# Performance work log

Measured on AMD Instinct MI355X. Metric: run time of the kernel, lower is better.

Reference implementation:

```python
import jax, jax.numpy as jnp
import numpy as np

N = 10000   # num_nodes (batch=1)
E = 160000  # num edges
CIN, H, T, OUT, K = 32, 64, 12, 12, 3


def _conv1d(x, w, b, pad):
    # x: [N, C_in, T], w: [C_out, C_in, K]
    out = jax.lax.conv_general_dilated(
        x, w, window_strides=(1,), padding=[(pad, pad)],
        dimension_numbers=('NCH', 'OIH', 'NCH'))
    return out + b[None, :, None]


def _gated_tconv(x, w, b):
    # GatedTemporalConv (dropout = identity in eval)
    out = _conv1d(x, w, b, K // 2)
    P, Q = jnp.split(out, 2, axis=1)
    return P * jax.nn.sigmoid(Q)


def _gcn(x, W, b, src, dst, ew):
    # PyG GCNConv, vectorized over all T timesteps in one fused pass.
    # x: [N, C_in, T], W: [C_out, C_in]
    xt = jnp.einsum('nct,oc->not', x, W)
    loop = jnp.arange(N)
    srcl = jnp.concatenate([src, loop])
    dstl = jnp.concatenate([dst, loop])
    ewl = jnp.concatenate([ew, jnp.ones((N,), ew.dtype)])
    deg = jax.ops.segment_sum(ewl, dstl, num_segments=N)
    dis = jnp.where(deg > 0, jax.lax.rsqrt(deg), 0.0)
    norm = dis[srcl] * ewl * dis[dstl]                      # [E+N]
    msg = xt[srcl] * norm[:, None, None]                    # [E+N, C_out, T]
    out = jax.ops.segment_sum(msg, dstl, num_segments=N)    # [N, C_out, T]
    return out + b[None, :, None]


def setup_inputs() -> dict:
    key = jax.random.key(0)
    ks = jax.random.split(key, 20)
    rn = lambda k, s: jax.random.normal(k, s, jnp.float32) * 0.05
    return {
        'x': jax.random.normal(ks[0], (N, CIN, T), jnp.float32),
        'edge_index': jax.random.randint(ks[1], (2, E), 0, N),
        'edge_weight': jax.random.uniform(ks[2], (E,), jnp.float32),
        'tc1a_w': rn(ks[3], (2 * H, CIN, K)), 'tc1a_b': rn(ks[4], (2 * H,)),
        'gc1_w': rn(ks[5], (H, H)),           'gc1_b': rn(ks[6], (H,)),
        'tc1b_w': rn(ks[7], (2 * H, H, K)),   'tc1b_b': rn(ks[8], (2 * H,)),
        'tc2a_w': rn(ks[9], (2 * H, H, K)),   'tc2a_b': rn(ks[10], (2 * H,)),
        'gc2_w': rn(ks[11], (H, H)),          'gc2_b': rn(ks[12], (H,)),
        'tc2b_w': rn(ks[13], (2 * H, H, K)),  'tc2b_b': rn(ks[14], (2 * H,)),
        'fin_w': rn(ks[15], (OUT, H, T)),     'fin_b': rn(ks[16], (OUT,)),
    }


def reference(x, edge_index, edge_weight,
              tc1a_w, tc1a_b, gc1_w, gc1_b, tc1b_w, tc1b_b,
              tc2a_w, tc2a_b, gc2_w, gc2_b, tc2b_w, tc2b_b,
              fin_w, fin_b):
    src, dst = edge_index[0], edge_index[1]
    h = _gated_tconv(x, tc1a_w, tc1a_b)
    h = jax.nn.relu(_gcn(h, gc1_w, gc1_b, src, dst, edge_weight))
    h = _gated_tconv(h, tc1b_w, tc1b_b)
    h = _gated_tconv(h, tc2a_w, tc2a_b)
    h = jax.nn.relu(_gcn(h, gc2_w, gc2_b, src, dst, edge_weight))
    h = _gated_tconv(h, tc2b_w, tc2b_b)
    h = _conv1d(h, fin_w, fin_b, 0)          # [N, OUT, 1] (kernel == T)
    h = h[:, :, 0]                            # squeeze(-1)
    return h.reshape(1, N, OUT)               # batch_size = 1
```

## Files before the change

kernel.cpp:

```cpp
#include <hip/hip_runtime.h>
#include <hip/hip_bf16.h>
#include <stdint.h>

#define N_NODES 10000
#define N_EDGES 160000

typedef unsigned short u16;
typedef unsigned int u32;
typedef short s16v8 __attribute__((ext_vector_type(8)));
typedef float f32v4 __attribute__((ext_vector_type(4)));

__device__ __forceinline__ float bf2f(u16 v){ return __uint_as_float(((u32)v) << 16); }
__device__ __forceinline__ float lo16(u32 u){ return __uint_as_float(u << 16); }
__device__ __forceinline__ float hi16(u32 u){ return __uint_as_float(u & 0xffff0000u); }
__device__ __forceinline__ u16 f2bf(float f){
    u32 u = __float_as_uint(f);
    u32 r = (u + 0x7fffu + ((u >> 16) & 1u)) >> 16;
    return (u16)r;
}
__device__ __forceinline__ u32 pack2(float a, float b){
    return (u32)f2bf(a) | ((u32)f2bf(b) << 16);
}

struct SmallPtrs { const void* p[14]; };

__device__ __constant__ const int g_seg_off[15] = {
    0, 12288, 12416, 16512, 16576, 41152, 41280,
    65856, 65984, 70080, 70144, 94720, 94848, 104064, 104076
};

__global__ void k_convert_init(SmallPtrs ps, u16* __restrict__ dst,
                               float* deg, int* cnt, int* cur){
    int i = blockIdx.x * blockDim.x + threadIdx.x;
    if (i < 104076){
        int seg = 0, base = 0;
#pragma unroll
        for (int s = 0; s < 14; s++){
            if (i >= g_seg_off[s]){ seg = s; base = g_seg_off[s]; }
        }
        dst[i] = f2bf(((const float*)ps.p[seg])[i - base]);
    }
    if (i < N_NODES){ deg[i] = 1.0f; cnt[i] = 0; cur[i] = 0; }
}

__global__ void k_graph_count(const int* __restrict__ ei, const float* __restrict__ ew,
                              float* deg, int* cnt){
    int e = blockIdx.x * blockDim.x + threadIdx.x;
    if (e < N_EDGES){
        int d = ei[N_EDGES + e];
        atomicAdd(&deg[d], ew[e]);
        atomicAdd(&cnt[d], 1);
    }
}

__global__ void k_scan_dis(const int* __restrict__ cnt, int* __restrict__ off,
                           const float* __restrict__ deg, float* __restrict__ dis){
    __shared__ int wsum[16], woff[16];
    int t = threadIdx.x;
    int lane = t & 63, wv = t >> 6;
    int base = t * 10;
    int loc[10];
    int mysum = 0;
    if (base < N_NODES){
#pragma unroll
        for (int j = 0; j < 10; j++){ loc[j] = mysum; mysum += cnt[base + j]; }
    }
    int s = mysum;
#pragma unroll
    for (int d = 1; d < 64; d <<= 1){
        int v = __shfl_up(s, d, 64);
        if (lane >= d) s += v;
    }
    if (lane == 63) wsum[wv] = s;
    __syncthreads();
    if (t < 16){
        int v = wsum[t];
        int sc = v;
#pragma unroll
        for (int d = 1; d < 16; d <<= 1){
            int u = __shfl_up(sc, d, 16);
            if (t >= d) sc += u;
        }
        woff[t] = sc - v;
        if (t == 15) off[N_NODES] = sc;
    }
    __syncthreads();
    int tbase = woff[wv] + (s - mysum);
    if (base < N_NODES){
#pragma unroll
        for (int j = 0; j < 10; j++) off[base + j] = tbase + loc[j];
    }
    for (int i = t; i < N_NODES; i += 1024) dis[i] = rsqrtf(deg[i]);
}

__global__ void k_scatter(const int* __restrict__ ei, const float* __restrict__ ew,
                          const float* __restrict__ dis, const int* __restrict__ off,
                          int* cur, int* __restrict__ esrc, float* __restrict__ enorm){
    int e = blockIdx.x * blockDim.x + threadIdx.x;
    if (e < N_EDGES){
        int s = ei[e];
        int d = ei[N_EDGES + e];
        float nw = dis[s] * ew[e] * dis[d];
        int p = off[d] + atomicAdd(&cur[d], 1);
        esrc[p] = s;
        enorm[p] = nw;
    }
}

__launch_bounds__(256, 2)
__global__ void k_gconv32(const float* __restrict__ xin, const u16* __restrict__ wg,
                          const u16* __restrict__ bg, u16* __restrict__ out){
    __shared__ __attribute__((aligned(16))) u16 xT[8][14][40];
    __shared__ __attribute__((aligned(16))) u16 Ho[8][12][72];
    int tid = threadIdx.x;
    int n0 = blockIdx.x * 8;

    for (int i = tid; i < 8 * 40; i += 256){
        int g = i / 40, c = i % 40;
        xT[g][0][c] = 0; xT[g][13][c] = 0;
    }
    {
        int g = tid >> 5, c = tid & 31;
        const float4* p = (const float4*)(xin + ((size_t)(n0 + g) * 32 + c) * 12);
        float4 v0 = p[0], v1 = p[1], v2 = p[2];
        xT[g][1][c] = f2bf(v0.x);  xT[g][2][c] = f2bf(v0.y);
        xT[g][3][c] = f2bf(v0.z);  xT[g][4][c] = f2bf(v0.w);
        xT[g][5][c] = f2bf(v1.x);  xT[g][6][c] = f2bf(v1.y);
        xT[g][7][c] = f2bf(v1.z);  xT[g][8][c] = f2bf(v1.w);
        xT[g][9][c] = f2bf(v2.x);  xT[g][10][c] = f2bf(v2.y);
        xT[g][11][c] = f2bf(v2.z); xT[g][12][c] = f2bf(v2.w);
    }
    int lane = tid & 63, wave = tid >> 6;
    int col = lane & 15, quad = lane >> 4;
    int o_p = wave * 16 + col, o_q = o_p + 64;

    s16v8 Bf[3][2];
#pragma unroll
    for (int pq = 0; pq < 2; pq++){
        const u16* wrow = wg + (size_t)(pq ? o_q : o_p) * 96;
#pragma unroll
        for (int d = 0; d < 3; d++){
            s16v8 b;
#pragma unroll
            for (int j = 0; j < 8; j++) b[j] = (short)wrow[(quad * 8 + j) * 3 + d];
            Bf[d][pq] = b;
        }
    }
    __syncthreads();

    f32v4 aP[6], aQ[6];
#pragma unroll
    for (int mt = 0; mt < 6; mt++){ aP[mt] = (f32v4)0.f; aQ[mt] = (f32v4)0.f; }
#pragma unroll
    for (int mt = 0; mt < 6; mt++){
        int m = mt * 16 + col;
        int g = m / 12, t = m - 12 * g;
#pragma unroll
        for (int d = 0; d < 3; d++){
            s16v8 a = *(const s16v8*)&xT[g][t + d][quad * 8];
            aP[mt] = __builtin_amdgcn_mfma_f32_16x16x32_bf16(a, Bf[d][0], aP[mt], 0, 0, 0);
            aQ[mt] = __builtin_amdgcn_mfma_f32_16x16x32_bf16(a, Bf[d][1], aQ[mt], 0, 0, 0);
        }
    }
    float bP = bf2f(bg[o_p]), bQ = bf2f(bg[o_q]);
#pragma unroll
    for (int mt = 0; mt < 6; mt++){
#pragma unroll
        for (int r = 0; r < 4; r++){
            int m2 = mt * 16 + quad * 4 + r;
            int g = m2 / 12, t = m2 - 12 * g;
            float pv = aP[mt][r] + bP, qv = aQ[mt][r] + bQ;
            Ho[g][t][o_p] = f2bf(pv / (1.f + __expf(-qv)));
        }
    }
    __syncthreads();
    for (int i = tid; i < 768; i += 256){
        int g = i / 96, r = i % 96, t = r / 8, ch = r % 8;
        *(s16v8*)(out + (size_t)(n0 + g) * 768 + t * 64 + ch * 8) = *(const s16v8*)&Ho[g][t][ch * 8];
    }
}

__global__ void k_agg(const u16* __restrict__ x, u16* __restrict__ out,
                      const float* __restrict__ dis, const int* __restrict__ off,
                      const int* __restrict__ esrc, const float* __restrict__ enorm){
    int n = blockIdx.x;
    int v0 = threadIdx.x * 4;
    float d = dis[n];
    float sw = d * d;
    const u16* xr = x + (size_t)n * 768 + v0;
    u32 u0 = *(const u32*)xr;
    u32 u1 = *(const u32*)(xr + 2);
    float a0 = sw * lo16(u0), a1 = sw * hi16(u0);
    float a2 = sw * lo16(u1), a3 = sw * hi16(u1);
    int b = off[n], e = off[n + 1];
    for (int p = b; p < e; p++){
        int s = esrc[p];
        float w = enorm[p];
        const u16* q = x + (size_t)s * 768 + v0;
        u32 w0 = *(const u32*)q;
        u32 w1 = *(const u32*)(q + 2);
        a0 = fmaf(w, lo16(w0), a0); a1 = fmaf(w, hi16(w0), a1);
        a2 = fmaf(w, lo16(w1), a2); a3 = fmaf(w, hi16(w1), a3);
    }
    u16* o = out + (size_t)n * 768 + v0;
    *(u32*)o       = pack2(a0, a1);
    *(u32*)(o + 2) = pack2(a2, a3);
}

#define XIDX(g, row, c) (((g) * 14 + (row)) * 72 + (c))

template<bool LAST>
__launch_bounds__(256, 2)
__global__ void k_fused(const u16* __restrict__ z,
                        const u16* __restrict__ Wmix, const u16* __restrict__ bmix,
                        const u16* __restrict__ w1, const u16* __restrict__ b1,
                        const u16* __restrict__ w2, const u16* __restrict__ b2,
                        const u16* __restrict__ fw, const u16* __restrict__ fb,
                        u16* __restrict__ outMid, float* __restrict__ outFin){
    __shared__ __attribute__((aligned(16))) u16 bufX[8 * 14 * 72];
    __shared__ __attribute__((aligned(16))) u16 bufY[8 * 14 * 72];
    int tid = threadIdx.x;
    int n0 = blockIdx.x * 8;
    int lane = tid & 63, wave = tid >> 6;
    int col = lane & 15, quad = lane >> 4;

    for (int i = tid; i < 8 * 72; i += 256){
        int g = i / 72, c = i % 72;
        bufX[XIDX(g, 0, c)] = 0; bufX[XIDX(g, 13, c)] = 0;
        bufY[XIDX(g, 0, c)] = 0; bufY[XIDX(g, 13, c)] = 0;
    }
    for (int i = tid; i < 768; i += 256){
        int g = i / 96, r = i % 96, t = r / 8, ch = r % 8;
        *(s16v8*)&bufX[XIDX(g, 1 + t, ch * 8)] =
            *(const s16v8*)(z + (size_t)(n0 + g) * 768 + t * 64 + ch * 8);
    }
    int o_mix = wave * 16 + col;
    s16v8 Bm[2];
#pragma unroll
    for (int ks = 0; ks < 2; ks++)
        Bm[ks] = *(const s16v8*)(Wmix + (size_t)o_mix * 64 + ks * 32 + quad * 8);
    __syncthreads();

    {
        f32v4 accm[6];
#pragma unroll
        for (int mt = 0; mt < 6; mt++) accm[mt] = (f32v4)0.f;
#pragma unroll
        for (int mt = 0; mt < 6; mt++){
            int m = mt * 16 + col;
            int g = m / 12, t = m - 12 * g;
#pragma unroll
            for (int ks = 0; ks < 2; ks++){
                s16v8 a = *(const s16v8*)&bufX[XIDX(g, 1 + t, ks * 32 + quad * 8)];
                accm[mt] = __builtin_amdgcn_mfma_f32_16x16x32_bf16(a, Bm[ks], accm[mt], 0, 0, 0);
            }
        }
        float bm = bf2f(bmix[o_mix]);
#pragma unroll
        for (int mt = 0; mt < 6; mt++){
#pragma unroll
            for (int r = 0; r < 4; r++){
                int m2 = mt * 16 + quad * 4 + r;
                int g = m2 / 12, t = m2 - 12 * g;
                bufY[XIDX(g, 1 + t, o_mix)] = f2bf(fmaxf(accm[mt][r] + bm, 0.f));
            }
        }
    }
    __syncthreads();

    {
        int o_p = wave * 16 + col, o_q = o_p + 64;
        s16v8 Bf[3][2][2];
#pragma unroll
        for (int pq = 0; pq < 2; pq++){
            const u16* wrow = w1 + (size_t)(pq ? o_q : o_p) * 192;
#pragma unroll
            for (int d = 0; d < 3; d++)
#pragma unroll
                for (int ks = 0; ks < 2; ks++){
                    s16v8 b;
#pragma unroll
                    for (int j = 0; j < 8; j++) b[j] = (short)wrow[(ks * 32 + quad * 8 + j) * 3 + d];
                    Bf[d][ks][pq] = b;
                }
        }
        f32v4 aP[6], aQ[6];
#pragma unroll
        for (int mt = 0; mt < 6; mt++){ aP[mt] = (f32v4)0.f; aQ[mt] = (f32v4)0.f; }
#pragma unroll
        for (int mt = 0; mt < 6; mt++){
            int m = mt * 16 + col;
            int g = m / 12, t = m - 12 * g;
#pragma unroll
            for (int d = 0; d < 3; d++)
#pragma unroll
                for (int ks = 0; ks < 2; ks++){
                    s16v8 a = *(const s16v8*)&bufY[XIDX(g, t + d, ks * 32 + quad * 8)];
                    aP[mt] = __builtin_amdgcn_mfma_f32_16x16x32_bf16(a, Bf[d][ks][0], aP[mt], 0, 0, 0);
                    aQ[mt] = __builtin_amdgcn_mfma_f32_16x16x32_bf16(a, Bf[d][ks][1], aQ[mt], 0, 0, 0);
                }
        }
        float bP = bf2f(b1[o_p]), bQ = bf2f(b1[o_q]);
#pragma unroll
        for (int mt = 0; mt < 6; mt++){
#pragma unroll
            for (int r = 0; r < 4; r++){
                int m2 = mt * 16 + quad * 4 + r;
                int g = m2 / 12, t = m2 - 12 * g;
                float pv = aP[mt][r] + bP, qv = aQ[mt][r] + bQ;
                u16 hv = f2bf(pv / (1.f + __expf(-qv)));
                if (LAST) bufX[g * 1008 + o_p * 12 + t] = hv;
                else      bufX[XIDX(g, 1 + t, o_p)] = hv;
            }
        }
    }
    __syncthreads();

    if (!LAST){
        int o_p = wave * 16 + col, o_q = o_p + 64;
        s16v8 Bf[3][2][2];
#pragma unroll
        for (int pq = 0; pq < 2; pq++){
            const u16* wrow = w2 + (size_t)(pq ? o_q : o_p) * 192;
#pragma unroll
            for (int d = 0; d < 3; d++)
#pragma unroll
                for (int ks = 0; ks < 2; ks++){
                    s16v8 b;
#pragma unroll
                    for (int j = 0; j < 8; j++) b[j] = (short)wrow[(ks * 32 + quad * 8 + j) * 3 + d];
                    Bf[d][ks][pq] = b;
                }
        }
        f32v4 aP[6], aQ[6];
#pragma unroll
        for (int mt = 0; mt < 6; mt++){ aP[mt] = (f32v4)0.f; aQ[mt] = (f32v4)0.f; }
#pragma unroll
        for (int mt = 0; mt < 6; mt++){
            int m = mt * 16 + col;
            int g = m / 12, t = m - 12 * g;
#pragma unroll
            for (int d = 0; d < 3; d++)
#pragma unroll
                for (int ks = 0; ks < 2; ks++){
                    s16v8 a = *(const s16v8*)&bufX[XIDX(g, t + d, ks * 32 + quad * 8)];
                    aP[mt] = __builtin_amdgcn_mfma_f32_16x16x32_bf16(a, Bf[d][ks][0], aP[mt], 0, 0, 0);
                    aQ[mt] = __builtin_amdgcn_mfma_f32_16x16x32_bf16(a, Bf[d][ks][1], aQ[mt], 0, 0, 0);
                }
        }
        float bP = bf2f(b2[o_p]), bQ = bf2f(b2[o_q]);
#pragma unroll
        for (int mt = 0; mt < 6; mt++){
#pragma unroll
            for (int r = 0; r < 4; r++){
                int m2 = mt * 16 + quad * 4 + r;
                int g = m2 / 12, t = m2 - 12 * g;
                float pv = aP[mt][r] + bP, qv = aQ[mt][r] + bQ;
                bufY[XIDX(g, 1 + t, o_p)] = f2bf(pv / (1.f + __expf(-qv)));
            }
        }
        __syncthreads();
        for (int i = tid; i < 768; i += 256){
            int g = i / 96, r = i % 96, t = r / 8, ch = r % 8;
            *(s16v8*)(outMid + (size_t)(n0 + g) * 768 + t * 64 + ch * 8) =
                *(const s16v8*)&bufY[XIDX(g, 1 + t, ch * 8)];
        }
    } else {
        if (wave == 0){
            f32v4 accF = {0.f, 0.f, 0.f, 0.f};
            int g8 = col & 7;
#pragma unroll
            for (int ks = 0; ks < 24; ks++){
                s16v8 a = *(const s16v8*)&bufX[g8 * 1008 + ks * 32 + quad * 8];
                s16v8 bfr = {0, 0, 0, 0, 0, 0, 0, 0};
                if (col < 12)
                    bfr = *(const s16v8*)(fw + (size_t)col * 768 + ks * 32 + quad * 8);
                accF = __builtin_amdgcn_mfma_f32_16x16x32_bf16(a, bfr, accF, 0, 0, 0);
            }
            if (col < 12){
                float bb = bf2f(fb[col]);
#pragma unroll
                for (int r = 0; r < 4; r++){
                    int g = quad * 4 + r;
                    if (g < 8) outFin[(size_t)(n0 + g) * 12 + col] = accF[r] + bb;
                }
            }
        }
    }
}

static inline size_t align256(size_t x){ return (x + 255) & ~(size_t)255; }

extern "C" void kernel_launch(void* const* d_in, const int* in_sizes, int n_in,
                              void* d_out, int out_size, void* d_ws, size_t ws_size,
                              hipStream_t stream){
    const float* x  = (const float*)d_in[0];
    const int* ei   = (const int*)d_in[1];
    const float* ew = (const float*)d_in[2];

    char* w = (char*)d_ws;
    u16* bufA    = (u16*)w;  w += align256((size_t)N_NODES * 768 * sizeof(u16));
    u16* bufB    = (u16*)w;  w += align256((size_t)N_NODES * 768 * sizeof(u16));
    float* deg   = (float*)w; w += align256(N_NODES * sizeof(float));
    float* dis   = (float*)w; w += align256(N_NODES * sizeof(float));
    int* cnt     = (int*)w;   w += align256(N_NODES * sizeof(int));
    int* off     = (int*)w;   w += align256((N_NODES + 1) * sizeof(int));
    int* cur     = (int*)w;   w += align256(N_NODES * sizeof(int));
    int* esrc    = (int*)w;   w += align256((size_t)N_EDGES * sizeof(int));
    float* enorm = (float*)w; w += align256((size_t)N_EDGES * sizeof(float));
    u16* cvt     = (u16*)w;   w += align256(104076 * sizeof(u16));

    u16* tc1a_w = cvt + 0;
    u16* tc1a_b = cvt + 12288;
    u16* gc1_w  = cvt + 12416;
    u16* gc1_b  = cvt + 16512;
    u16* tc1b_w = cvt + 16576;
    u16* tc1b_b = cvt + 41152;
    u16* tc2a_w = cvt + 41280;
    u16* tc2a_b = cvt + 65856;
    u16* gc2_w  = cvt + 65984;
    u16* gc2_b  = cvt + 70080;
    u16* tc2b_w = cvt + 70144;
    u16* tc2b_b = cvt + 94720;
    u16* fin_w  = cvt + 94848;
    u16* fin_b  = cvt + 104064;

    SmallPtrs ps;
    ps.p[0]  = d_in[3];  ps.p[1]  = d_in[4];
    ps.p[2]  = d_in[5];  ps.p[3]  = d_in[6];
    ps.p[4]  = d_in[7];  ps.p[5]  = d_in[8];
    ps.p[6]  = d_in[9];  ps.p[7]  = d_in[10];
    ps.p[8]  = d_in[11]; ps.p[9]  = d_in[12];
    ps.p[10] = d_in[13]; ps.p[11] = d_in[14];
    ps.p[12] = d_in[15]; ps.p[13] = d_in[16];

    k_convert_init<<<(104076 + 255) / 256, 256, 0, stream>>>(ps, cvt, deg, cnt, cur);
    k_graph_count<<<(N_EDGES + 255) / 256, 256, 0, stream>>>(ei, ew, deg, cnt);
    k_scan_dis<<<1, 1024, 0, stream>>>(cnt, off, deg, dis);
    k_scatter<<<(N_EDGES + 255) / 256, 256, 0, stream>>>(ei, ew, dis, off, cur, esrc, enorm);

    k_gconv32<<<1250, 256, 0, stream>>>(x, tc1a_w, tc1a_b, bufA);
    k_agg<<<N_NODES, 192, 0, stream>>>(bufA, bufB, dis, off, esrc, enorm);
    k_fused<false><<<1250, 256, 0, stream>>>(bufB, gc1_w, gc1_b, tc1b_w, tc1b_b,
                                             tc2a_w, tc2a_b, nullptr, nullptr,
                                             bufA, nullptr);
    k_agg<<<N_NODES, 192, 0, stream>>>(bufA, bufB, dis, off, esrc, enorm);
    k_fused<true><<<1250, 256, 0, stream>>>(bufB, gc2_w, gc2_b, tc2b_w, tc2b_b,
                                            nullptr, nullptr, fin_w, fin_b,
                                            nullptr, (float*)d_out);
}
```

Measured before the change: 274.3 us.

## Fuse graph aggregation into fused conv kernels and merge count with first conv

Removes the separate k_agg kernels and performs the neighbor aggregation at the start of each k_fused block, writing the aggregated rows straight into shared memory and skipping a global round-trip. The degree counting is merged into the first gated conv launch as extra blocks, and edge source and weight are packed into int2. The conv weights are pre-transposed at conversion time so each B fragment loads as one vector. The cost is lower aggregation parallelism, since one thread now gathers 24 contiguous values per node. Register pressure also rises in k_fused.

Measured after the change: 266.6 us. -2.8%, faster.

```diff
diff --git a/kernel.cpp b/kernel.cpp
--- a/kernel.cpp
+++ b/kernel.cpp
@@ -11,22 +11,20 @@
 typedef float f32v4 __attribute__((ext_vector_type(4)));
 
 __device__ __forceinline__ float bf2f(u16 v){ return __uint_as_float(((u32)v) << 16); }
-__device__ __forceinline__ float lo16(u32 u){ return __uint_as_float(u << 16); }
-__device__ __forceinline__ float hi16(u32 u){ return __uint_as_float(u & 0xffff0000u); }
 __device__ __forceinline__ u16 f2bf(float f){
     u32 u = __float_as_uint(f);
     u32 r = (u + 0x7fffu + ((u >> 16) & 1u)) >> 16;
     return (u16)r;
 }
-__device__ __forceinline__ u32 pack2(float a, float b){
-    return (u32)f2bf(a) | ((u32)f2bf(b) << 16);
-}
 
 struct SmallPtrs { const void* p[14]; };
 
 __device__ __constant__ const int g_seg_off[15] = {
     0, 12288, 12416, 16512, 16576, 41152, 41280,
     65856, 65984, 70080, 70144, 94720, 94848, 104064, 104076
+};
+__device__ __constant__ const int g_seg_kind[14] = {
+    1, 0, 0, 0, 2, 0, 2, 0, 0, 0, 2, 0, 0, 0
 };
 
 __global__ void k_convert_init(SmallPtrs ps, u16* __restrict__ dst,
@@ -38,78 +36,36 @@
         for (int s = 0; s < 14; s++){
             if (i >= g_seg_off[s]){ seg = s; base = g_seg_off[s]; }
         }
-        dst[i] = f2bf(((const float*)ps.p[seg])[i - base]);
+        int li = i - base;
+        float v = ((const float*)ps.p[seg])[li];
+        int kind = g_seg_kind[seg];
+        int dsto = li;
+        if (kind){
+            int CIN = (kind == 1) ? 32 : 64;
+            int o = li / (3 * CIN);
+            int rem = li - o * (3 * CIN);
+            int c = rem / 3, d = rem - c * 3;
+            dsto = d * 128 * CIN + o * CIN + c;
+        }
+        dst[base + dsto] = f2bf(v);
     }
     if (i < N_NODES){ deg[i] = 1.0f; cnt[i] = 0; cur[i] = 0; }
 }
 
-__global__ void k_graph_count(const int* __restrict__ ei, const float* __restrict__ ew,
+__launch_bounds__(256, 2)
+__global__ void k_gconv_count(const float* __restrict__ xin, const u16* __restrict__ wg,
+                              const u16* __restrict__ bg, u16* __restrict__ out,
+                              const int* __restrict__ ei, const float* __restrict__ ew,
                               float* deg, int* cnt){
-    int e = blockIdx.x * blockDim.x + threadIdx.x;
-    if (e < N_EDGES){
-        int d = ei[N_EDGES + e];
-        atomicAdd(&deg[d], ew[e]);
-        atomicAdd(&cnt[d], 1);
-    }
-}
-
-__global__ void k_scan_dis(const int* __restrict__ cnt, int* __restrict__ off,
-                           const float* __restrict__ deg, float* __restrict__ dis){
-    __shared__ int wsum[16], woff[16];
-    int t = threadIdx.x;
-    int lane = t & 63, wv = t >> 6;
-    int base = t * 10;
-    int loc[10];
-    int mysum = 0;
-    if (base < N_NODES){
-#pragma unroll
-        for (int j = 0; j < 10; j++){ loc[j] = mysum; mysum += cnt[base + j]; }
-    }
-    int s = mysum;
-#pragma unroll
-    for (int d = 1; d < 64; d <<= 1){
-        int v = __shfl_up(s, d, 64);
-        if (lane >= d) s += v;
-    }
-    if (lane == 63) wsum[wv] = s;
-    __syncthreads();
-    if (t < 16){
-        int v = wsum[t];
-        int sc = v;
-#pragma unroll
-        for (int d = 1; d < 16; d <<= 1){
-            int u = __shfl_up(sc, d, 16);
-            if (t >= d) sc += u;
-        }
-        woff[t] = sc - v;
-        if (t == 15) off[N_NODES] = sc;
-    }
-    __syncthreads();
-    int tbase = woff[wv] + (s - mysum);
-    if (base < N_NODES){
-#pragma unroll
-        for (int j = 0; j < 10; j++) off[base + j] = tbase + loc[j];
-    }
-    for (int i = t; i < N_NODES; i += 1024) dis[i] = rsqrtf(deg[i]);
-}
-
-__global__ void k_scatter(const int* __restrict__ ei, const float* __restrict__ ew,
-                          const float* __restrict__ dis, const int* __restrict__ off,
-                          int* cur, int* __restrict__ esrc, float* __restrict__ enorm){
-    int e = blockIdx.x * blockDim.x + threadIdx.x;
-    if (e < N_EDGES){
-        int s = ei[e];
-        int d = ei[N_EDGES + e];
-        float nw = dis[s] * ew[e] * dis[d];
-        int p = off[d] + atomicAdd(&cur[d], 1);
-        esrc[p] = s;
-        enorm[p] = nw;
-    }
-}
-
-__launch_bounds__(256, 2)
-__global__ void k_gconv32(const float* __restrict__ xin, const u16* __restrict__ wg,
-                          const u16* __restrict__ bg, u16* __restrict__ out){
+    if (blockIdx.x >= 1250){
+        int e = (blockIdx.x - 1250) * 256 + threadIdx.x;
+        if (e < N_EDGES){
+            int d = ei[N_EDGES + e];
+            atomicAdd(&deg[d], ew[e]);
+            atomicAdd(&cnt[d], 1);
+        }
+        return;
+    }
     __shared__ __attribute__((aligned(16))) u16 xT[8][14][40];
     __shared__ __attribute__((aligned(16))) u16 Ho[8][12][72];
     int tid = threadIdx.x;
@@ -137,14 +93,10 @@
     s16v8 Bf[3][2];
 #pragma unroll
     for (int pq = 0; pq < 2; pq++){
-        const u16* wrow = wg + (size_t)(pq ? o_q : o_p) * 96;
-#pragma unroll
-        for (int d = 0; d < 3; d++){
-            s16v8 b;
-#pragma unroll
-            for (int j = 0; j < 8; j++) b[j] = (short)wrow[(quad * 8 + j) * 3 + d];
-            Bf[d][pq] = b;
-        }
+        int o = pq ? o_q : o_p;
+#pragma unroll
+        for (int d = 0; d < 3; d++)
+            Bf[d][pq] = *(const s16v8*)(wg + d * 4096 + o * 32 + quad * 8);
     }
     __syncthreads();
 
@@ -180,38 +132,66 @@
     }
 }
 
-__global__ void k_agg(const u16* __restrict__ x, u16* __restrict__ out,
-                      const float* __restrict__ dis, const int* __restrict__ off,
-                      const int* __restrict__ esrc, const float* __restrict__ enorm){
-    int n = blockIdx.x;
-    int v0 = threadIdx.x * 4;
-    float d = dis[n];
-    float sw = d * d;
-    const u16* xr = x + (size_t)n * 768 + v0;
-    u32 u0 = *(const u32*)xr;
-    u32 u1 = *(const u32*)(xr + 2);
-    float a0 = sw * lo16(u0), a1 = sw * hi16(u0);
-    float a2 = sw * lo16(u1), a3 = sw * hi16(u1);
-    int b = off[n], e = off[n + 1];
-    for (int p = b; p < e; p++){
-        int s = esrc[p];
-        float w = enorm[p];
-        const u16* q = x + (size_t)s * 768 + v0;
-        u32 w0 = *(const u32*)q;
-        u32 w1 = *(const u32*)(q + 2);
-        a0 = fmaf(w, lo16(w0), a0); a1 = fmaf(w, hi16(w0), a1);
-        a2 = fmaf(w, lo16(w1), a2); a3 = fmaf(w, hi16(w1), a3);
-    }
-    u16* o = out + (size_t)n * 768 + v0;
-    *(u32*)o       = pack2(a0, a1);
-    *(u32*)(o + 2) = pack2(a2, a3);
+__global__ void k_scan_dis(const int* __restrict__ cnt, int* __restrict__ off,
+                           const float* __restrict__ deg, float* __restrict__ dis){
+    __shared__ int wsum[16], woff[16];
+    int t = threadIdx.x;
+    int lane = t & 63, wv = t >> 6;
+    int base = t * 10;
+    int loc[10];
+    int mysum = 0;
+    if (base < N_NODES){
+#pragma unroll
+        for (int j = 0; j < 10; j++){ loc[j] = mysum; mysum += cnt[base + j]; }
+    }
+    int s = mysum;
+#pragma unroll
+    for (int d = 1; d < 64; d <<= 1){
+        int v = __shfl_up(s, d, 64);
+        if (lane >= d) s += v;
+    }
+    if (lane == 63) wsum[wv] = s;
+    __syncthreads();
+    if (t < 16){
+        int v = wsum[t];
+        int sc = v;
+#pragma unroll
+        for (int d = 1; d < 16; d <<= 1){
+            int u = __shfl_up(sc, d, 16);
+            if (t >= d) sc += u;
+        }
+        woff[t] = sc - v;
+        if (t == 15) off[N_NODES] = sc;
+    }
+    __syncthreads();
+    int tbase = woff[wv] + (s - mysum);
+    if (base < N_NODES){
+#pragma unroll
+        for (int j = 0; j < 10; j++) off[base + j] = tbase + loc[j];
+    }
+    for (int i = t; i < N_NODES; i += 1024) dis[i] = rsqrtf(deg[i]);
+}
+
+__global__ void k_scatter(const int* __restrict__ ei, const float* __restrict__ ew,
+                          const float* __restrict__ dis, const int* __restrict__ off,
+                          int* cur, int2* __restrict__ epack){
+    int e = blockIdx.x * blockDim.x + threadIdx.x;
+    if (e < N_EDGES){
+        int s = ei[e];
+        int d = ei[N_EDGES + e];
+        float nw = dis[s] * ew[e] * dis[d];
+        int p = off[d] + atomicAdd(&cur[d], 1);
+        epack[p] = make_int2(s, __float_as_int(nw));
+    }
 }
 
 #define XIDX(g, row, c) (((g) * 14 + (row)) * 72 + (c))
 
 template<bool LAST>
 __launch_bounds__(256, 2)
-__global__ void k_fused(const u16* __restrict__ z,
+__global__ void k_fused(const u16* __restrict__ src,
+                        const float* __restrict__ dis, const int* __restrict__ off,
+                        const int2* __restrict__ ep,
                         const u16* __restrict__ Wmix, const u16* __restrict__ bmix,
                         const u16* __restrict__ w1, const u16* __restrict__ b1,
                         const u16* __restrict__ w2, const u16* __restrict__ b2,
@@ -229,11 +209,43 @@
         bufX[XIDX(g, 0, c)] = 0; bufX[XIDX(g, 13, c)] = 0;
         bufY[XIDX(g, 0, c)] = 0; bufY[XIDX(g, 13, c)] = 0;
     }
-    for (int i = tid; i < 768; i += 256){
-        int g = i / 96, r = i % 96, t = r / 8, ch = r % 8;
-        *(s16v8*)&bufX[XIDX(g, 1 + t, ch * 8)] =
-            *(const s16v8*)(z + (size_t)(n0 + g) * 768 + t * 64 + ch * 8);
-    }
+
+    {
+        int g = tid >> 5, j = tid & 31;
+        int n = n0 + g;
+        float dv = dis[n];
+        float sw = dv * dv;
+        const u16* xr = src + (size_t)n * 768 + j * 24;
+        float acc[24];
+#pragma unroll
+        for (int k = 0; k < 3; k++){
+            s16v8 v = *(const s16v8*)(xr + k * 8);
+#pragma unroll
+            for (int q = 0; q < 8; q++) acc[k * 8 + q] = sw * bf2f((u16)v[q]);
+        }
+        int b = off[n], e = off[n + 1];
+        for (int p = b; p < e; p++){
+            int2 pr = ep[p];
+            float w = __int_as_float(pr.y);
+            const u16* qr = src + (size_t)pr.x * 768 + j * 24;
+#pragma unroll
+            for (int k = 0; k < 3; k++){
+                s16v8 v = *(const s16v8*)(qr + k * 8);
+#pragma unroll
+                for (int q = 0; q < 8; q++) acc[k * 8 + q] = fmaf(w, bf2f((u16)v[q]), acc[k * 8 + q]);
+            }
+        }
+#pragma unroll
+        for (int k = 0; k < 3; k++){
+            int flat = j * 24 + k * 8;
+            int t = flat >> 6, c = flat & 63;
+            s16v8 hv;
+#pragma unroll
+            for (int q = 0; q < 8; q++) hv[q] = (short)f2bf(acc[k * 8 + q]);
+            *(s16v8*)&bufX[XIDX(g, 1 + t, c)] = hv;
+        }
+    }
+
     int o_mix = wave * 16 + col;
     s16v8 Bm[2];
 #pragma unroll
@@ -273,16 +285,12 @@
         s16v8 Bf[3][2][2];
 #pragma unroll
         for (int pq = 0; pq < 2; pq++){
-            const u16* wrow = w1 + (size_t)(pq ? o_q : o_p) * 192;
+            int o = pq ? o_q : o_p;
 #pragma unroll
             for (int d = 0; d < 3; d++)
 #pragma unroll
-                for (int ks = 0; ks < 2; ks++){
-                    s16v8 b;
-#pragma unroll
-                    for (int j = 0; j < 8; j++) b[j] = (short)wrow[(ks * 32 + quad * 8 + j) * 3 + d];
-                    Bf[d][ks][pq] = b;
-                }
+                for (int ks = 0; ks < 2; ks++)
+                    Bf[d][ks][pq] = *(const s16v8*)(w1 + d * 8192 + o * 64 + ks * 32 + quad * 8);
         }
         f32v4 aP[6], aQ[6];
 #pragma unroll
@@ -321,16 +329,12 @@
         s16v8 Bf[3][2][2];
 #pragma unroll
         for (int pq = 0; pq < 2; pq++){
-            const u16* wrow = w2 + (size_t)(pq ? o_q : o_p) * 192;
+            int o = pq ? o_q : o_p;
 #pragma unroll
             for (int d = 0; d < 3; d++)
 #pragma unroll
-                for (int ks = 0; ks < 2; ks++){
-                    s16v8 b;
-#pragma unroll
-                    for (int j = 0; j < 8; j++) b[j] = (short)wrow[(ks * 32 + quad * 8 + j) * 3 + d];
-                    Bf[d][ks][pq] = b;
-                }
+                for (int ks = 0; ks < 2; ks++)
+                    Bf[d][ks][pq] = *(const s16v8*)(w2 + d * 8192 + o * 64 + ks * 32 + quad * 8);
         }
         f32v4 aP[6], aQ[6];
 #pragma unroll
@@ -406,8 +410,7 @@
     int* cnt     = (int*)w;   w += align256(N_NODES * sizeof(int));
     int* off     = (int*)w;   w += align256((N_NODES + 1) * sizeof(int));
     int* cur     = (int*)w;   w += align256(N_NODES * sizeof(int));
-    int* esrc    = (int*)w;   w += align256((size_t)N_EDGES * sizeof(int));
-    float* enorm = (float*)w; w += align256((size_t)N_EDGES * sizeof(float));
+    int2* epack  = (int2*)w;  w += align256((size_t)N_EDGES * sizeof(int2));
     u16* cvt     = (u16*)w;   w += align256(104076 * sizeof(u16));
 
     u16* tc1a_w = cvt + 0;
@@ -435,17 +438,16 @@
     ps.p[12] = d_in[15]; ps.p[13] = d_in[16];
 
     k_convert_init<<<(104076 + 255) / 256, 256, 0, stream>>>(ps, cvt, deg, cnt, cur);
-    k_graph_count<<<(N_EDGES + 255) / 256, 256, 0, stream>>>(ei, ew, deg, cnt);
+    k_gconv_count<<<1250 + 625, 256, 0, stream>>>(x, tc1a_w, tc1a_b, bufA, ei, ew, deg, cnt);
     k_scan_dis<<<1, 1024, 0, stream>>>(cnt, off, deg, dis);
-    k_scatter<<<(N_EDGES + 255) / 256, 256, 0, stream>>>(ei, ew, dis, off, cur, esrc, enorm);
-
-    k_gconv32<<<1250, 256, 0, stream>>>(x, tc1a_w, tc1a_b, bufA);
-    k_agg<<<N_NODES, 192, 0, stream>>>(bufA, bufB, dis, off, esrc, enorm);
-    k_fused<false><<<1250, 256, 0, stream>>>(bufB, gc1_w, gc1_b, tc1b_w, tc1b_b,
+    k_scatter<<<625, 256, 0, stream>>>(ei, ew, dis, off, cur, epack);
+
+    k_fused<false><<<1250, 256, 0, stream>>>(bufA, dis, off, epack,
+                                             gc1_w, gc1_b, tc1b_w, tc1b_b,
                                              tc2a_w, tc2a_b, nullptr, nullptr,
-                                             bufA, nullptr);
-    k_agg<<<N_NODES, 192, 0, stream>>>(bufA, bufB, dis, off, esrc, enorm);
-    k_fused<true><<<1250, 256, 0, stream>>>(bufB, gc2_w, gc2_b, tc2b_w, tc2b_b,
+                                             bufB, nullptr);
+    k_fused<true><<<1250, 256, 0, stream>>>(bufB, dis, off, epack,
+                                            gc2_w, gc2_b, tc2b_w, tc2b_b,
                                             nullptr, nullptr, fin_w, fin_b,
                                             nullptr, (float*)d_out);
 }
```
